# Optimization experiments

Hardware: AMD Instinct MI355X
Metric: run time of the kernel (lower is better)

The kernel has to match this reference:

```python
import jax, jax.numpy as jnp
import numpy as np

B, S, IN_DIM, CTX = 32, 512, 256, 128
D, H, L = 128, 4, 2
DH = D // H
HID = 512
TOTAL = 11 * D * D + 8 * D  # hypernet flat weight size per sample
EPS = 1e-5


def _layernorm(x, g, b):
    mu = jnp.mean(x, axis=-1, keepdims=True)
    var = jnp.mean(jnp.square(x - mu), axis=-1, keepdims=True)
    return (x - mu) * jax.lax.rsqrt(var + EPS) * g + b


def setup_inputs() -> dict:
    key = jax.random.key(0)
    ks = jax.random.split(key, 24)
    f32 = jnp.float32
    inp = {
        'x': jax.random.normal(ks[0], (B, S, IN_DIM), f32),
        'context_vector': jax.random.normal(ks[1], (B, CTX), f32),
        'in_proj_w': jax.random.normal(ks[2], (D, IN_DIM), f32) * (IN_DIM ** -0.5),
        'in_proj_b': jnp.zeros((D,), f32),
        'pe': jax.random.normal(ks[3], (1, S, D), f32) * 0.02,
        'hfc1_w': jax.random.normal(ks[4], (L, HID, CTX), f32) * (CTX ** -0.5),
        'hfc1_b': jnp.zeros((L, HID), f32),
        'hfc2_w': jax.random.normal(ks[5], (L, TOTAL, HID), f32) * 0.02,
        'hfc2_b': jnp.zeros((L, TOTAL), f32),
        'out_proj_w': jax.random.normal(ks[6], (L, D, D), f32) * (D ** -0.5),
        'out_proj_b': jnp.zeros((L, D), f32),
        'ln1_g': jnp.ones((L, D), f32), 'ln1_b': jnp.zeros((L, D), f32),
        'ln2_g': jnp.ones((L, D), f32), 'ln2_b': jnp.zeros((L, D), f32),
        'alpha1': jnp.full((L,), 0.5, f32), 'alpha2': jnp.full((L,), 0.5, f32),
        'head_w': jax.random.normal(ks[7], (1, D), f32) * (D ** -0.5),
        'head_b': jnp.zeros((1,), f32),
    }
    return inp


def reference(x, context_vector, in_proj_w, in_proj_b, pe, hfc1_w, hfc1_b,
              hfc2_w, hfc2_b, out_proj_w, out_proj_b, ln1_g, ln1_b,
              ln2_g, ln2_b, alpha1, alpha2, head_w, head_b):
    # input projection + learned positional encoding
    h = jnp.einsum('bsi,di->bsd', x, in_proj_w) + in_proj_b
    h = h + pe[:, :h.shape[1], :]

    # flat split offsets for hypernet output
    sizes = [3 * D * D, 3 * D, 4 * D * D, 4 * D, 4 * D * D, D]
    offs = np.concatenate([[0], np.cumsum(sizes)])

    for l in range(L):
        # hypernet: per-sample weights from context
        hid = jax.nn.relu(context_vector @ hfc1_w[l].T + hfc1_b[l])
        flat = hid @ hfc2_w[l].T + hfc2_b[l]  # [B, TOTAL]
        aw = flat[:, offs[0]:offs[1]].reshape(B, 3 * D, D)
        ab = flat[:, offs[1]:offs[2]]                     # [B, 3D]
        f1w = flat[:, offs[2]:offs[3]].reshape(B, 4 * D, D)
        f1b = flat[:, offs[3]:offs[4]]                    # [B, 4D]
        f2w = flat[:, offs[4]:offs[5]].reshape(B, D, 4 * D)
        f2b = flat[:, offs[5]:offs[6]]                    # [B, D]

        # per-sample QKV projection (grouped GEMM over batch)
        qkv = jnp.einsum('bsd,bed->bse', h, aw) + ab[:, None, :]
        q, k, v = jnp.split(qkv, 3, axis=-1)
        q = q.reshape(B, S, H, DH)
        k = k.reshape(B, S, H, DH)
        v = v.reshape(B, S, H, DH)
        scores = jnp.einsum('bqhd,bkhd->bhqk', q, k) / jnp.sqrt(jnp.float32(DH))
        attn = jax.nn.softmax(scores, axis=-1)
        ctx = jnp.einsum('bhqk,bkhd->bqhd', attn, v).reshape(B, S, D)
        attn_out = jnp.einsum('bsd,ed->bse', ctx, out_proj_w[l]) + out_proj_b[l]

        h = _layernorm(h + alpha1[l] * attn_out, ln1_g[l], ln1_b[l])

        # per-sample FFN
        ff = jax.nn.relu(jnp.einsum('bsd,bfd->bsf', h, f1w) + f1b[:, None, :])
        ff = jnp.einsum('bsf,bdf->bsd', ff, f2w) + f2b[:, None, :]

        h = _layernorm(h + alpha2[l] * ff, ln2_g[l], ln2_b[l])

    out = h[:, -1, :] @ head_w.T + head_b  # [B, 1]
    return out
```

## Files before the change

kernel.cpp:

```cpp
#include <hip/hip_runtime.h>
#include <hip/hip_bf16.h>

constexpr int B_    = 32;
constexpr int S_    = 512;
constexpr int INDIM = 256;
constexpr int KCTX  = 128;
constexpr int D_    = 128;
constexpr int H_    = 4;
constexpr int L_    = 2;
constexpr int HID_  = 512;
constexpr int TOTAL_ = 11 * D_ * D_ + 8 * D_;
constexpr int OFF_AB  = 3 * D_ * D_;
constexpr int OFF_F1W = OFF_AB + 3 * D_;
constexpr int OFF_F1B = OFF_F1W + 4 * D_ * D_;
constexpr int OFF_F2W = OFF_F1B + 4 * D_;
constexpr int OFF_F2B = OFF_F2W + 4 * D_ * D_;

typedef __attribute__((ext_vector_type(8))) short short8;
typedef __attribute__((ext_vector_type(4))) short short4v;
typedef __attribute__((ext_vector_type(2))) short short2v;
typedef __attribute__((ext_vector_type(4))) float f32x4;

#define MFMA16 __builtin_amdgcn_mfma_f32_16x16x32_bf16

__device__ __forceinline__ short f2bf(float f) {
  __hip_bfloat16 h = __float2bfloat16(f);
  return __builtin_bit_cast(short, h);
}
__device__ __forceinline__ float bf2f(short s) {
  __hip_bfloat16 h = __builtin_bit_cast(__hip_bfloat16, s);
  return __bfloat162float(h);
}
struct bfpair { short hi, lo; };
__device__ __forceinline__ bfpair split2p(float x) {
  bfpair p;
  p.hi = f2bf(x);
  p.lo = f2bf(x - bf2f(p.hi));
  return p;
}

__device__ __forceinline__ long ftaddr(int row, int k, int K) {
  return ((long)(row >> 4) * (K >> 3) + (k >> 3)) * 128 + (row & 15) * 8 + (k & 7);
}

__global__ void k_cvtft(const float* __restrict__ in, short* __restrict__ oh,
                        short* __restrict__ ol, int ktShift, int n8) {
  int t = blockIdx.x * 256 + threadIdx.x;
  if (t >= n8) return;
  int kt = 1 << ktShift;
  int row = t >> ktShift;
  int kc = t & (kt - 1);
  const float* p = in + ((long)row << (ktShift + 3)) + kc * 8;
  float4 v0 = *(const float4*)p;
  float4 v1 = *(const float4*)(p + 4);
  short8 h8, l8;
  bfpair q;
  q = split2p(v0.x); h8[0] = q.hi; l8[0] = q.lo;
  q = split2p(v0.y); h8[1] = q.hi; l8[1] = q.lo;
  q = split2p(v0.z); h8[2] = q.hi; l8[2] = q.lo;
  q = split2p(v0.w); h8[3] = q.hi; l8[3] = q.lo;
  q = split2p(v1.x); h8[4] = q.hi; l8[4] = q.lo;
  q = split2p(v1.y); h8[5] = q.hi; l8[5] = q.lo;
  q = split2p(v1.z); h8[6] = q.hi; l8[6] = q.lo;
  q = split2p(v1.w); h8[7] = q.hi; l8[7] = q.lo;
  long o = ((long)(row >> 4) * kt + kc) * 128 + (row & 15) * 8;
  *(short8*)(oh + o) = h8;
  *(short8*)(ol + o) = l8;
}

__global__ __launch_bounds__(512) void k_hid(const float* __restrict__ cvec,
                                             const float* __restrict__ w,
                                             const float* __restrict__ bias,
                                             short* __restrict__ hh,
                                             short* __restrict__ hl) {
  int lb = blockIdx.x;
  int b  = lb & 31;
  int j  = threadIdx.x;
  __shared__ float cs[KCTX];
  if (j < KCTX) cs[j] = cvec[b * KCTX + j];
  __syncthreads();
  int l = lb >> 5;
  const float* wr = w + (long)(l * HID_ + j) * KCTX;
  float s = bias[l * HID_ + j];
  #pragma unroll
  for (int c = 0; c < KCTX; c += 4) {
    float4 cv = *(const float4*)(cs + c);
    float4 wv = *(const float4*)(wr + c);
    s += cv.x * wv.x + cv.y * wv.y + cv.z * wv.z + cv.w * wv.w;
  }
  s = fmaxf(s, 0.f);
  bfpair p = split2p(s);
  long o = (long)l * 32 * HID_ + ((long)(b >> 4) * 64 + (j >> 3)) * 128 + (b & 15) * 8 + (j & 7);
  hh[o] = p.hi;
  hl[o] = p.lo;
}

__device__ __forceinline__ void store_flat(int b, int trow, float v,
    short* __restrict__ awh, short* __restrict__ awl,
    short* __restrict__ f1h, short* __restrict__ f1l,
    short* __restrict__ f2h, short* __restrict__ f2l,
    float* __restrict__ ab, float* __restrict__ f1b, float* __restrict__ f2b) {
  if (trow < OFF_AB) {
    int e = trow >> 7, d = trow & 127;
    long a = (long)b * 49152 + ftaddr(e, d, 128);
    bfpair p = split2p(v); awh[a] = p.hi; awl[a] = p.lo;
  } else if (trow < OFF_F1W) {
    ab[b * 384 + trow - OFF_AB] = v;
  } else if (trow < OFF_F1B) {
    int i = trow - OFF_F1W; int f = i >> 7, d = i & 127;
    long a = (long)b * 65536 + ftaddr(f, d, 128);
    bfpair p = split2p(v); f1h[a] = p.hi; f1l[a] = p.lo;
  } else if (trow < OFF_F2W) {
    f1b[b * 512 + trow - OFF_F1B] = v;
  } else if (trow < OFF_F2B) {
    int i = trow - OFF_F2W; int dd = i >> 9, f = i & 511;
    long a = (long)b * 65536 + ftaddr(dd, f, 512);
    bfpair p = split2p(v); f2h[a] = p.hi; f2l[a] = p.lo;
  } else {
    f2b[b * 128 + trow - OFF_F2B] = v;
  }
}

__global__ __launch_bounds__(256) void k_flat(
    const short* __restrict__ hidh, const short* __restrict__ hidl,
    const float* __restrict__ W, const float* __restrict__ bias,
    short* __restrict__ awh, short* __restrict__ awl,
    short* __restrict__ f1h, short* __restrict__ f1l,
    short* __restrict__ f2h, short* __restrict__ f2l,
    float* __restrict__ ab, float* __restrict__ f1b, float* __restrict__ f2b) {
  __shared__ short wls[2][64 * 64];
  const int tid = threadIdx.x, wave = tid >> 6, lane = tid & 63;
  const int r = lane & 15, g = lane >> 4;
  const int nb0 = blockIdx.x * 64;
  const int rr = tid >> 4;
  const int cc = (tid & 15) * 4;
  const float* wbase = W + (long)nb0 * HID_;
  float4 wv[2][4];
  #pragma unroll
  for (int rnd = 0; rnd < 4; ++rnd) {
    wv[0][rnd] = *(const float4*)(wbase + (long)(rnd * 16 + rr) * HID_ + cc);
    wv[1][rnd] = *(const float4*)(wbase + (long)(rnd * 16 + rr) * HID_ + 64 + cc);
  }
  const short* pAh = hidh + g * 128 + r * 8;
  const short* pAl = hidl + g * 128 + r * 8;
  f32x4 acc0 = {0, 0, 0, 0}, acc1 = {0, 0, 0, 0};
  int cur = 0;
  for (int c0 = 0; c0 < 512; c0 += 64) {
    #pragma unroll
    for (int rnd = 0; rnd < 4; ++rnd) {
      int row = rnd * 16 + rr;
      short4v h4, l4; bfpair q;
      q = split2p(wv[cur][rnd].x); h4[0] = q.hi; l4[0] = q.lo;
      q = split2p(wv[cur][rnd].y); h4[1] = q.hi; l4[1] = q.lo;
      q = split2p(wv[cur][rnd].z); h4[2] = q.hi; l4[2] = q.lo;
      q = split2p(wv[cur][rnd].w); h4[3] = q.hi; l4[3] = q.lo;
      int sb = row * 128 + ((cc * 2) ^ ((row & 7) << 4));
      *(short4v*)((char*)&wls[0][0] + sb) = h4;
      *(short4v*)((char*)&wls[1][0] + sb) = l4;
    }
    if (c0 + 128 < 512) {
      #pragma unroll
      for (int rnd = 0; rnd < 4; ++rnd)
        wv[cur][rnd] = *(const float4*)(wbase + (long)(rnd * 16 + rr) * HID_ + (c0 + 128) + cc);
    }
    __syncthreads();
    #pragma unroll
    for (int kk = 0; kk < 2; ++kk) {
      long ao = (long)(c0 * 16) + kk * 512;
      short8 ah0 = *(const short8*)(pAh + ao);
      short8 ah1 = *(const short8*)(pAh + 8192 + ao);
      short8 al0 = *(const short8*)(pAl + ao);
      short8 al1 = *(const short8*)(pAl + 8192 + ao);
      int wrow = wave * 16 + r;
      int wb = wrow * 128 + ((kk * 64 + g * 16) ^ ((r & 7) << 4));
      short8 wh = *(const short8*)((char*)&wls[0][0] + wb);
      short8 wl = *(const short8*)((char*)&wls[1][0] + wb);
      acc0 = MFMA16(ah0, wl, acc0, 0, 0, 0);
      acc0 = MFMA16(al0, wh, acc0, 0, 0, 0);
      acc0 = MFMA16(ah0, wh, acc0, 0, 0, 0);
      acc1 = MFMA16(ah1, wl, acc1, 0, 0, 0);
      acc1 = MFMA16(al1, wh, acc1, 0, 0, 0);
      acc1 = MFMA16(ah1, wh, acc1, 0, 0, 0);
    }
    __syncthreads();
    cur ^= 1;
  }
  int trow = nb0 + wave * 16 + r;
  float bv = bias[trow];
  #pragma unroll
  for (int reg = 0; reg < 4; ++reg) {
    store_flat(g * 4 + reg, trow, acc0[reg] + bv, awh, awl, f1h, f1l, f2h, f2l, ab, f1b, f2b);
    store_flat(g * 4 + reg + 16, trow, acc1[reg] + bv, awh, awl, f1h, f1l, f2h, f2l, ab, f1b, f2b);
  }
}

template <int K, int EPI, bool RELU>
__global__ __launch_bounds__(256) void k_gemm(
    const short* __restrict__ Ah, const short* __restrict__ Al, long sA,
    const short* __restrict__ Wh, const short* __restrict__ Wl, long sW,
    const float* __restrict__ biasP, long sB,
    void* __restrict__ p0, void* __restrict__ p1,
    void* __restrict__ p2, void* __restrict__ p3,
    const float* __restrict__ pe, int N,
    const float* __restrict__ lng, const float* __restrict__ lnb,
    const float* __restrict__ lnal) {
  extern __shared__ char smem_dyn[];
  const int tid = threadIdx.x, wave = tid >> 6, lane = tid & 63;
  const int r = lane & 15, g = lane >> 4;
  const int b = blockIdx.z;
  const int m0 = blockIdx.x * 64 + (wave & 1) * 32;
  const int n0 = blockIdx.y * 128 + (wave >> 1) * 64;
  const long KT = (long)K * 16;
  const short* pAh = Ah + (long)b * sA + (m0 >> 4) * KT + g * 128 + r * 8;
  const short* pAl = Al + (long)b * sA + (m0 >> 4) * KT + g * 128 + r * 8;
  const short* pWh = Wh + (long)b * sW + (n0 >> 4) * KT + g * 128 + r * 8;
  const short* pWl = Wl + (long)b * sW + (n0 >> 4) * KT + g * 128 + r * 8;
  f32x4 acc[2][4] = {{{0,0,0,0},{0,0,0,0},{0,0,0,0},{0,0,0,0}},
                     {{0,0,0,0},{0,0,0,0},{0,0,0,0},{0,0,0,0}}};
  for (int kk = 0; kk < K / 32; ++kk) {
    long ko = (long)kk * 512;
    short8 a0h = *(const short8*)(pAh + ko);
    short8 a1h = *(const short8*)(pAh + KT + ko);
    short8 a0l = *(const short8*)(pAl + ko);
    short8 a1l = *(const short8*)(pAl + KT + ko);
    #pragma unroll
    for (int ns = 0; ns < 4; ++ns) {
      short8 wh = *(const short8*)(pWh + ns * KT + ko);
      short8 wl = *(const short8*)(pWl + ns * KT + ko);
      acc[0][ns] = MFMA16(a0h, wl, acc[0][ns], 0, 0, 0);
      acc[0][ns] = MFMA16(a0l, wh, acc[0][ns], 0, 0, 0);
      acc[0][ns] = MFMA16(a0h, wh, acc[0][ns], 0, 0, 0);
      acc[1][ns] = MFMA16(a1h, wl, acc[1][ns], 0, 0, 0);
      acc[1][ns] = MFMA16(a1l, wh, acc[1][ns], 0, 0, 0);
      acc[1][ns] = MFMA16(a1h, wh, acc[1][ns], 0, 0, 0);
    }
  }
  #pragma unroll
  for (int ms = 0; ms < 2; ++ms) {
    #pragma unroll
    for (int ns = 0; ns < 4; ++ns) {
      int ccol = n0 + ns * 16 + r;
      float bv = biasP[(long)b * sB + ccol];
      #pragma unroll
      for (int reg = 0; reg < 4; ++reg) {
        int crow = m0 + ms * 16 + g * 4 + reg;
        float v = acc[ms][ns][reg] + bv;
        if constexpr (RELU) v = fmaxf(v, 0.f);
        if constexpr (EPI == 0) {
          long o = (long)b * 512 * N + (long)(crow >> 4) * (N * 16)
                 + (long)(ccol >> 3) * 128 + (crow & 15) * 8 + (ccol & 7);
          bfpair sp = split2p(v);
          ((short*)p0)[o] = sp.hi;
          ((short*)p1)[o] = sp.lo;
        } else if constexpr (EPI == 1) {
          v += pe[crow * D_ + ccol];
          ((float*)p0)[((long)b * S_ + crow) * D_ + ccol] = v;
          long o = (long)b * 65536 + (long)(crow >> 4) * 2048
                 + (ccol >> 3) * 128 + (crow & 15) * 8 + (ccol & 7);
          bfpair sp = split2p(v);
          ((short*)p1)[o] = sp.hi;
          ((short*)p2)[o] = sp.lo;
        } else if constexpr (EPI == 4) {
          float* tile = (float*)smem_dyn;
          int trow2 = (wave & 1) * 32 + ms * 16 + g * 4 + reg;
          int tcol = (wave >> 1) * 64 + ns * 16 + r;
          tile[trow2 * 136 + tcol] = v;
        } else {
          bfpair sp = split2p(v);
          if (n0 < 256) {
            long o = (long)b * 131072 + (long)(crow >> 4) * 4096
                   + (ccol >> 3) * 128 + (crow & 15) * 8 + (ccol & 7);
            ((short*)p0)[o] = sp.hi;
            ((short*)p1)[o] = sp.lo;
          } else {
            int c2 = ccol - 256; int hd = c2 >> 5, dd = c2 & 31;
            long o = (long)(b * 4 + hd) * 16384 + (dd >> 4) * 8192
                   + (crow >> 3) * 128 + (dd & 15) * 8 + (crow & 7);
            ((short*)p2)[o] = sp.hi;
            ((short*)p3)[o] = sp.lo;
          }
        }
      }
    }
  }
  if constexpr (EPI == 4) {
    float* tile = (float*)smem_dyn;
    __syncthreads();
    int row = tid >> 2, q = tid & 3;
    int brow = blockIdx.x * 64 + row;
    float a = lnal[0];
    float* hf = (float*)p0;
    float* hrow = hf + ((long)b * S_ + brow) * D_ + q * 32;
    float tv[32];
    float s = 0.f, ss = 0.f;
    #pragma unroll
    for (int i = 0; i < 32; i += 4) {
      float4 hv = *(const float4*)(hrow + i);
      float4 yv = *(const float4*)&tile[row * 136 + q * 32 + i];
      float t0 = hv.x + a * yv.x, t1 = hv.y + a * yv.y;
      float t2 = hv.z + a * yv.z, t3 = hv.w + a * yv.w;
      tv[i] = t0; tv[i+1] = t1; tv[i+2] = t2; tv[i+3] = t3;
      s += t0 + t1 + t2 + t3;
      ss += t0*t0 + t1*t1 + t2*t2 + t3*t3;
    }
    s  += __shfl_xor(s, 1);  s  += __shfl_xor(s, 2);
    ss += __shfl_xor(ss, 1); ss += __shfl_xor(ss, 2);
    float mu = s * (1.f / 128.f);
    float varv = ss * (1.f / 128.f) - mu * mu;
    float inv = rsqrtf(varv + 1e-5f);
    short* ph = (short*)p1; short* pl = (short*)p2;
    long fb = (long)b * 65536 + (long)(brow >> 4) * 2048 + (brow & 15) * 8;
    #pragma unroll
    for (int j = 0; j < 4; ++j) {
      short8 hv8, lv8;
      #pragma unroll
      for (int e = 0; e < 8; e += 4) {
        int i = j * 8 + e;
        int c = q * 32 + i;
        float4 gv = *(const float4*)(lng + c);
        float4 bb = *(const float4*)(lnb + c);
        float4 o4;
        o4.x = (tv[i]   - mu) * inv * gv.x + bb.x;
        o4.y = (tv[i+1] - mu) * inv * gv.y + bb.y;
        o4.z = (tv[i+2] - mu) * inv * gv.z + bb.z;
        o4.w = (tv[i+3] - mu) * inv * gv.w + bb.w;
        *(float4*)(hrow + i) = o4;
        bfpair q0 = split2p(o4.x); hv8[e]   = q0.hi; lv8[e]   = q0.lo;
        bfpair q1 = split2p(o4.y); hv8[e+1] = q1.hi; lv8[e+1] = q1.lo;
        bfpair q2 = split2p(o4.z); hv8[e+2] = q2.hi; lv8[e+2] = q2.lo;
        bfpair q3 = split2p(o4.w); hv8[e+3] = q3.hi; lv8[e+3] = q3.lo;
      }
      long o = fb + (q * 4 + j) * 128;
      *(short8*)(ph + o) = hv8;
      *(short8*)(pl + o) = lv8;
    }
  }
}

__global__ __launch_bounds__(128) void k_attn(const short* __restrict__ qkh,
                                              const short* __restrict__ qkl,
                                              const short* __restrict__ vth,
                                              const short* __restrict__ vtl,
                                              short* __restrict__ ch,
                                              short* __restrict__ cl) {
  __shared__ __align__(16) float scr[16][516];
  __shared__ __align__(16) float obuf[16][34];
  const int tid = threadIdx.x, wave = tid >> 6, lane = tid & 63;
  const int r = lane & 15, g = lane >> 4;
  const int b = blockIdx.z, hh = blockIdx.y;
  const int m0 = blockIdx.x * 16;
  const long qb = (long)b * 131072;
  const long qoff = qb + (long)(m0 >> 4) * 4096 + (hh * 4 + g) * 128 + r * 8;
  short8 qh = *(const short8*)(qkh + qoff);
  short8 ql = *(const short8*)(qkl + qoff);
  const float sc = 0.17677669529663687f;
  for (int n0 = wave * 256; n0 < wave * 256 + 256; n0 += 16) {
    long koff = qb + (long)(n0 >> 4) * 4096 + (16 + hh * 4 + g) * 128 + r * 8;
    short8 kh = *(const short8*)(qkh + koff);
    short8 kl = *(const short8*)(qkl + koff);
    f32x4 s = {0, 0, 0, 0};
    s = MFMA16(qh, kl, s, 0, 0, 0);
    s = MFMA16(ql, kh, s, 0, 0, 0);
    s = MFMA16(qh, kh, s, 0, 0, 0);
    #pragma unroll
    for (int reg = 0; reg < 4; ++reg)
      scr[g * 4 + reg][n0 + r] = s[reg] * sc;
  }
  __syncthreads();
  for (int row = wave * 8; row < wave * 8 + 8; ++row) {
    float v[8];
    #pragma unroll
    for (int i = 0; i < 8; ++i) v[i] = scr[row][lane + i * 64];
    float m = v[0];
    #pragma unroll
    for (int i = 1; i < 8; ++i) m = fmaxf(m, v[i]);
    #pragma unroll
    for (int o = 32; o > 0; o >>= 1) m = fmaxf(m, __shfl_xor(m, o));
    float ssum = 0.f;
    #pragma unroll
    for (int i = 0; i < 8; ++i) { v[i] = __expf(v[i] - m); ssum += v[i]; }
    #pragma unroll
    for (int o = 32; o > 0; o >>= 1) ssum += __shfl_xor(ssum, o);
    float inv = 1.f / ssum;
    #pragma unroll
    for (int i = 0; i < 8; ++i) scr[row][lane + i * 64] = v[i] * inv;
  }
  __syncthreads();
  f32x4 o0 = {0, 0, 0, 0}, o1 = {0, 0, 0, 0};
  const long vb = (long)(b * 4 + hh) * 16384;
  for (int kt = wave * 8; kt < wave * 8 + 8; ++kt) {
    float4 pv0 = *(const float4*)&scr[r][kt * 32 + g * 8];
    float4 pv1 = *(const float4*)&scr[r][kt * 32 + g * 8 + 4];
    short8 pah, pal;
    bfpair p;
    p = split2p(pv0.x); pah[0] = p.hi; pal[0] = p.lo;
    p = split2p(pv0.y); pah[1] = p.hi; pal[1] = p.lo;
    p = split2p(pv0.z); pah[2] = p.hi; pal[2] = p.lo;
    p = split2p(pv0.w); pah[3] = p.hi; pal[3] = p.lo;
    p = split2p(pv1.x); pah[4] = p.hi; pal[4] = p.lo;
    p = split2p(pv1.y); pah[5] = p.hi; pal[5] = p.lo;
    p = split2p(pv1.z); pah[6] = p.hi; pal[6] = p.lo;
    p = split2p(pv1.w); pah[7] = p.hi; pal[7] = p.lo;
    long vo = vb + (long)(kt * 4 + g) * 128 + r * 8;
    short8 vh0 = *(const short8*)(vth + vo);
    short8 vh1 = *(const short8*)(vth + vo + 8192);
    short8 vl0 = *(const short8*)(vtl + vo);
    short8 vl1 = *(const short8*)(vtl + vo + 8192);
    o0 = MFMA16(pah, vl0, o0, 0, 0, 0);
    o0 = MFMA16(pal, vh0, o0, 0, 0, 0);
    o0 = MFMA16(pah, vh0, o0, 0, 0, 0);
    o1 = MFMA16(pah, vl1, o1, 0, 0, 0);
    o1 = MFMA16(pal, vh1, o1, 0, 0, 0);
    o1 = MFMA16(pah, vh1, o1, 0, 0, 0);
  }
  if (wave == 1) {
    #pragma unroll
    for (int reg = 0; reg < 4; ++reg) {
      obuf[g * 4 + reg][r] = o0[reg];
      obuf[g * 4 + reg][17 + r] = o1[reg];
    }
  }
  __syncthreads();
  if (wave == 0) {
    #pragma unroll
    for (int reg = 0; reg < 4; ++reg) {
      float a0 = o0[reg] + obuf[g * 4 + reg][r];
      float a1 = o1[reg] + obuf[g * 4 + reg][17 + r];
      int srow = m0 + g * 4 + reg;
      int col0 = hh * 32 + r;
      long o = (long)b * 65536 + (long)(srow >> 4) * 2048
             + (col0 >> 3) * 128 + (srow & 15) * 8 + (col0 & 7);
      bfpair sp0 = split2p(a0);
      ch[o] = sp0.hi; cl[o] = sp0.lo;
      long o2 = o + 2 * 128;
      bfpair sp1 = split2p(a1);
      ch[o2] = sp1.hi; cl[o2] = sp1.lo;
    }
  }
}

__global__ __launch_bounds__(64) void k_head(const float* __restrict__ h,
                                             const float* __restrict__ hw,
                                             const float* __restrict__ hb,
                                             float* __restrict__ out) {
  int b = blockIdx.x, lane = threadIdx.x;
  const float* hr = h + ((long)b * S_ + (S_ - 1)) * D_;
  float v = hr[lane] * hw[lane] + hr[lane + 64] * hw[lane + 64];
  #pragma unroll
  for (int o = 32; o > 0; o >>= 1) v += __shfl_xor(v, o);
  if (lane == 0) out[b] = v + hb[0];
}

extern "C" void kernel_launch(void* const* d_in, const int* in_sizes, int n_in,
                              void* d_out, int out_size, void* d_ws, size_t ws_size,
                              hipStream_t stream) {
  const float* x    = (const float*)d_in[0];
  const float* cvec = (const float*)d_in[1];
  const float* ipw  = (const float*)d_in[2];
  const float* ipb  = (const float*)d_in[3];
  const float* pe   = (const float*)d_in[4];
  const float* h1w  = (const float*)d_in[5];
  const float* h1b  = (const float*)d_in[6];
  const float* h2w  = (const float*)d_in[7];
  const float* h2b  = (const float*)d_in[8];
  const float* opw  = (const float*)d_in[9];
  const float* opb  = (const float*)d_in[10];
  const float* ln1g = (const float*)d_in[11];
  const float* ln1b = (const float*)d_in[12];
  const float* ln2g = (const float*)d_in[13];
  const float* ln2b = (const float*)d_in[14];
  const float* a1   = (const float*)d_in[15];
  const float* a2   = (const float*)d_in[16];
  const float* hw   = (const float*)d_in[17];
  const float* hb   = (const float*)d_in[18];
  float* out = (float*)d_out;

  char* ws = (char*)d_ws;
  size_t off = 0;
  auto alloc = [&](size_t n) { void* p = ws + off; off = (off + n + 255) & ~(size_t)255; return p; };

  short* ff1h  = (short*)alloc((size_t)B_ * S_ * 512 * 2);
  short* ff1l  = (short*)alloc((size_t)B_ * S_ * 512 * 2);
  short* xFh   = ff1h;
  short* xFl   = ff1l;
  float* h_f   = (float*)alloc((size_t)B_ * S_ * D_ * 4);
  short* hFh   = (short*)alloc((size_t)B_ * S_ * D_ * 2);
  short* hFl   = (short*)alloc((size_t)B_ * S_ * D_ * 2);
  short* hidFh = (short*)alloc((size_t)L_ * 32 * HID_ * 2);
  short* hidFl = (short*)alloc((size_t)L_ * 32 * HID_ * 2);
  short* awFh  = (short*)alloc((size_t)B_ * 49152 * 2);
  short* awFl  = (short*)alloc((size_t)B_ * 49152 * 2);
  short* f1wFh = (short*)alloc((size_t)B_ * 65536 * 2);
  short* f1wFl = (short*)alloc((size_t)B_ * 65536 * 2);
  short* f2wFh = (short*)alloc((size_t)B_ * 65536 * 2);
  short* f2wFl = (short*)alloc((size_t)B_ * 65536 * 2);
  float* abF   = (float*)alloc((size_t)B_ * 384 * 4);
  float* f1bF  = (float*)alloc((size_t)B_ * 512 * 4);
  float* f2bF  = (float*)alloc((size_t)B_ * 128 * 4);
  short* qkFh  = (short*)alloc((size_t)B_ * S_ * 256 * 2);
  short* qkFl  = (short*)alloc((size_t)B_ * S_ * 256 * 2);
  short* vtFh  = (short*)alloc((size_t)B_ * H_ * 32 * S_ * 2);
  short* vtFl  = (short*)alloc((size_t)B_ * H_ * 32 * S_ * 2);
  short* cxFh  = (short*)alloc((size_t)B_ * S_ * D_ * 2);
  short* cxFl  = (short*)alloc((size_t)B_ * S_ * D_ * 2);
  short* ipwFh = (short*)alloc((size_t)D_ * INDIM * 2);
  short* ipwFl = (short*)alloc((size_t)D_ * INDIM * 2);
  short* opwFh = (short*)alloc((size_t)L_ * D_ * D_ * 2);
  short* opwFl = (short*)alloc((size_t)L_ * D_ * D_ * 2);

  k_cvtft<<<(B_ * S_ * INDIM / 8 + 255) / 256, 256, 0, stream>>>(x, xFh, xFl, 5, B_ * S_ * INDIM / 8);
  k_cvtft<<<16, 256, 0, stream>>>(ipw, ipwFh, ipwFl, 5, D_ * INDIM / 8);
  k_cvtft<<<16, 256, 0, stream>>>(opw, opwFh, opwFl, 4, L_ * D_ * D_ / 8);

  k_hid<<<L_ * 32, 512, 0, stream>>>(cvec, h1w, h1b, hidFh, hidFl);

  k_gemm<INDIM, 1, false><<<dim3(8, 1, B_), 256, 0, stream>>>(
      xFh, xFl, (long)S_ * INDIM, ipwFh, ipwFl, 0, ipb, 0,
      h_f, hFh, hFl, nullptr, pe, 128, nullptr, nullptr, nullptr);

  constexpr size_t LN_LDS = 64 * 136 * 4;
  for (int l = 0; l < L_; ++l) {
    k_flat<<<TOTAL_ / 64, 256, 0, stream>>>(
        hidFh + (long)l * 32 * HID_, hidFl + (long)l * 32 * HID_,
        h2w + (long)l * TOTAL_ * HID_, h2b + (long)l * TOTAL_,
        awFh, awFl, f1wFh, f1wFl, f2wFh, f2wFl, abF, f1bF, f2bF);
    k_gemm<D_, 5, false><<<dim3(8, 3, B_), 256, 0, stream>>>(
        hFh, hFl, (long)S_ * D_, awFh, awFl, 49152, abF, 384,
        qkFh, qkFl, vtFh, vtFl, nullptr, 256, nullptr, nullptr, nullptr);
    k_attn<<<dim3(S_ / 16, H_, B_), 128, 0, stream>>>(qkFh, qkFl, vtFh, vtFl, cxFh, cxFl);
    k_gemm<D_, 4, false><<<dim3(8, 1, B_), 256, LN_LDS, stream>>>(
        cxFh, cxFl, (long)S_ * D_, opwFh + l * 16384, opwFl + l * 16384, 0,
        opb + l * D_, 0, h_f, hFh, hFl, nullptr, nullptr, 128,
        ln1g + l * D_, ln1b + l * D_, a1 + l);
    k_gemm<D_, 0, true><<<dim3(8, 4, B_), 256, 0, stream>>>(
        hFh, hFl, (long)S_ * D_, f1wFh, f1wFl, 65536, f1bF, 512,
        ff1h, ff1l, nullptr, nullptr, nullptr, 512, nullptr, nullptr, nullptr);
    k_gemm<512, 4, false><<<dim3(8, 1, B_), 256, LN_LDS, stream>>>(
        ff1h, ff1l, (long)S_ * 512, f2wFh, f2wFl, 65536, f2bF, 128,
        h_f, hFh, hFl, nullptr, nullptr, 128,
        ln2g + l * D_, ln2b + l * D_, a2 + l);
  }
  k_head<<<B_, 64, 0, stream>>>(h_f, hw, hb, out);
}
```

Before: 513.1 us.

## Load hypernet weights directly into MFMA fragments, dropping LDS staging and barriers

The hypernet output GEMM kernel no longer stages fp32 weight tiles through shared memory with swizzling and two barriers per chunk. Each lane now loads its own 8 contiguous weights per K-step straight from global memory, with a one-step register prefetch, splits them into bf16 hi/lo, and feeds them to the MFMAs. This removes LDS traffic and synchronisation in a kernel that streams a large weight matrix once. The cost is less coalesced global access: each lane reads 32 bytes from a separate row, so every access touches many rows at once.

```diff
diff --git a/kernel.cpp b/kernel.cpp
--- a/kernel.cpp
+++ b/kernel.cpp
@@ -128,69 +128,55 @@
     short* __restrict__ f1h, short* __restrict__ f1l,
     short* __restrict__ f2h, short* __restrict__ f2l,
     float* __restrict__ ab, float* __restrict__ f1b, float* __restrict__ f2b) {
-  __shared__ short wls[2][64 * 64];
   const int tid = threadIdx.x, wave = tid >> 6, lane = tid & 63;
   const int r = lane & 15, g = lane >> 4;
   const int nb0 = blockIdx.x * 64;
-  const int rr = tid >> 4;
-  const int cc = (tid & 15) * 4;
-  const float* wbase = W + (long)nb0 * HID_;
-  float4 wv[2][4];
-  #pragma unroll
-  for (int rnd = 0; rnd < 4; ++rnd) {
-    wv[0][rnd] = *(const float4*)(wbase + (long)(rnd * 16 + rr) * HID_ + cc);
-    wv[1][rnd] = *(const float4*)(wbase + (long)(rnd * 16 + rr) * HID_ + 64 + cc);
-  }
+  const int wrow = nb0 + wave * 16 + r;
+  const float* wp = W + (long)wrow * HID_ + g * 8;
   const short* pAh = hidh + g * 128 + r * 8;
   const short* pAl = hidl + g * 128 + r * 8;
   f32x4 acc0 = {0, 0, 0, 0}, acc1 = {0, 0, 0, 0};
-  int cur = 0;
-  for (int c0 = 0; c0 < 512; c0 += 64) {
-    #pragma unroll
-    for (int rnd = 0; rnd < 4; ++rnd) {
-      int row = rnd * 16 + rr;
-      short4v h4, l4; bfpair q;
-      q = split2p(wv[cur][rnd].x); h4[0] = q.hi; l4[0] = q.lo;
-      q = split2p(wv[cur][rnd].y); h4[1] = q.hi; l4[1] = q.lo;
-      q = split2p(wv[cur][rnd].z); h4[2] = q.hi; l4[2] = q.lo;
-      q = split2p(wv[cur][rnd].w); h4[3] = q.hi; l4[3] = q.lo;
-      int sb = row * 128 + ((cc * 2) ^ ((row & 7) << 4));
-      *(short4v*)((char*)&wls[0][0] + sb) = h4;
-      *(short4v*)((char*)&wls[1][0] + sb) = l4;
-    }
-    if (c0 + 128 < 512) {
-      #pragma unroll
-      for (int rnd = 0; rnd < 4; ++rnd)
-        wv[cur][rnd] = *(const float4*)(wbase + (long)(rnd * 16 + rr) * HID_ + (c0 + 128) + cc);
-    }
-    __syncthreads();
-    #pragma unroll
-    for (int kk = 0; kk < 2; ++kk) {
-      long ao = (long)(c0 * 16) + kk * 512;
-      short8 ah0 = *(const short8*)(pAh + ao);
-      short8 ah1 = *(const short8*)(pAh + 8192 + ao);
-      short8 al0 = *(const short8*)(pAl + ao);
-      short8 al1 = *(const short8*)(pAl + 8192 + ao);
-      int wrow = wave * 16 + r;
-      int wb = wrow * 128 + ((kk * 64 + g * 16) ^ ((r & 7) << 4));
-      short8 wh = *(const short8*)((char*)&wls[0][0] + wb);
-      short8 wl = *(const short8*)((char*)&wls[1][0] + wb);
-      acc0 = MFMA16(ah0, wl, acc0, 0, 0, 0);
-      acc0 = MFMA16(al0, wh, acc0, 0, 0, 0);
-      acc0 = MFMA16(ah0, wh, acc0, 0, 0, 0);
-      acc1 = MFMA16(ah1, wl, acc1, 0, 0, 0);
-      acc1 = MFMA16(al1, wh, acc1, 0, 0, 0);
-      acc1 = MFMA16(ah1, wh, acc1, 0, 0, 0);
-    }
-    __syncthreads();
-    cur ^= 1;
-  }
-  int trow = nb0 + wave * 16 + r;
-  float bv = bias[trow];
+  float4 w0 = *(const float4*)(wp);
+  float4 w1 = *(const float4*)(wp + 4);
+  short8 ah0 = *(const short8*)(pAh);
+  short8 ah1 = *(const short8*)(pAh + 8192);
+  short8 al0 = *(const short8*)(pAl);
+  short8 al1 = *(const short8*)(pAl + 8192);
+  #pragma unroll
+  for (int kk = 0; kk < 16; ++kk) {
+    float4 cw0 = w0, cw1 = w1;
+    short8 ch0 = ah0, ch1 = ah1, cl0 = al0, cl1 = al1;
+    if (kk < 15) {
+      long wo = (long)(kk + 1) * 32;
+      w0 = *(const float4*)(wp + wo);
+      w1 = *(const float4*)(wp + wo + 4);
+      long ao = (long)(kk + 1) * 512;
+      ah0 = *(const short8*)(pAh + ao);
+      ah1 = *(const short8*)(pAh + 8192 + ao);
+      al0 = *(const short8*)(pAl + ao);
+      al1 = *(const short8*)(pAl + 8192 + ao);
+    }
+    short8 wh, wl; bfpair q;
+    q = split2p(cw0.x); wh[0] = q.hi; wl[0] = q.lo;
+    q = split2p(cw0.y); wh[1] = q.hi; wl[1] = q.lo;
+    q = split2p(cw0.z); wh[2] = q.hi; wl[2] = q.lo;
+    q = split2p(cw0.w); wh[3] = q.hi; wl[3] = q.lo;
+    q = split2p(cw1.x); wh[4] = q.hi; wl[4] = q.lo;
+    q = split2p(cw1.y); wh[5] = q.hi; wl[5] = q.lo;
+    q = split2p(cw1.z); wh[6] = q.hi; wl[6] = q.lo;
+    q = split2p(cw1.w); wh[7] = q.hi; wl[7] = q.lo;
+    acc0 = MFMA16(ch0, wl, acc0, 0, 0, 0);
+    acc0 = MFMA16(cl0, wh, acc0, 0, 0, 0);
+    acc0 = MFMA16(ch0, wh, acc0, 0, 0, 0);
+    acc1 = MFMA16(ch1, wl, acc1, 0, 0, 0);
+    acc1 = MFMA16(cl1, wh, acc1, 0, 0, 0);
+    acc1 = MFMA16(ch1, wh, acc1, 0, 0, 0);
+  }
+  float bv = bias[wrow];
   #pragma unroll
   for (int reg = 0; reg < 4; ++reg) {
-    store_flat(g * 4 + reg, trow, acc0[reg] + bv, awh, awl, f1h, f1l, f2h, f2l, ab, f1b, f2b);
-    store_flat(g * 4 + reg + 16, trow, acc1[reg] + bv, awh, awl, f1h, f1l, f2h, f2l, ab, f1b, f2b);
+    store_flat(g * 4 + reg, wrow, acc0[reg] + bv, awh, awl, f1h, f1l, f2h, f2l, ab, f1b, f2b);
+    store_flat(g * 4 + reg + 16, wrow, acc1[reg] + bv, awh, awl, f1h, f1l, f2h, f2l, ab, f1b, f2b);
   }
 }
 
```

Measured after the change: 558.2 us. 1.09x slower.

## Batch both hypernet layers in one launch and vectorize GEMM epilogue stores

Applied to the files above, without the earlier changes.

The two per-layer hypernet weight-generation launches become one launch with a layer grid dimension, and the generated weights are stored per layer in larger workspace buffers. The GEMM epilogue for the QKV and FFN1 outputs now stages results through an LDS tile and writes 8-wide vectorized bf16 hi/lo stores instead of scattered scalar stores. The V-transpose part is written with 4-wide vector stores. The LDS tile pitch changes from 136 to 132 floats. This adds LDS traffic and a barrier to those GEMMs and doubles the weight workspace.

```diff
diff --git a/kernel.cpp b/kernel.cpp
--- a/kernel.cpp
+++ b/kernel.cpp
@@ -15,6 +15,7 @@
 constexpr int OFF_F1B = OFF_F1W + 4 * D_ * D_;
 constexpr int OFF_F2W = OFF_F1B + 4 * D_;
 constexpr int OFF_F2B = OFF_F2W + 4 * D_ * D_;
+constexpr int TP = 132;
 
 typedef __attribute__((ext_vector_type(8))) short short8;
 typedef __attribute__((ext_vector_type(4))) short short4v;
@@ -129,6 +130,15 @@
     short* __restrict__ f2h, short* __restrict__ f2l,
     float* __restrict__ ab, float* __restrict__ f1b, float* __restrict__ f2b) {
   __shared__ short wls[2][64 * 64];
+  const int l = blockIdx.y;
+  hidh += (long)l * 32 * HID_;
+  hidl += (long)l * 32 * HID_;
+  W    += (long)l * TOTAL_ * HID_;
+  bias += (long)l * TOTAL_;
+  awh  += (long)l * B_ * 49152;  awl += (long)l * B_ * 49152;
+  f1h  += (long)l * B_ * 65536;  f1l += (long)l * B_ * 65536;
+  f2h  += (long)l * B_ * 65536;  f2l += (long)l * B_ * 65536;
+  ab   += l * B_ * 384;  f1b += l * B_ * 512;  f2b += l * B_ * 128;
   const int tid = threadIdx.x, wave = tid >> 6, lane = tid & 63;
   const int r = lane & 15, g = lane >> 4;
   const int nb0 = blockIdx.x * 64;
@@ -235,57 +245,99 @@
       acc[1][ns] = MFMA16(a1h, wh, acc[1][ns], 0, 0, 0);
     }
   }
-  #pragma unroll
-  for (int ms = 0; ms < 2; ++ms) {
-    #pragma unroll
-    for (int ns = 0; ns < 4; ++ns) {
-      int ccol = n0 + ns * 16 + r;
-      float bv = biasP[(long)b * sB + ccol];
+
+  if constexpr (EPI == 5) {
+    if (blockIdx.y == 2) {
       #pragma unroll
-      for (int reg = 0; reg < 4; ++reg) {
-        int crow = m0 + ms * 16 + g * 4 + reg;
-        float v = acc[ms][ns][reg] + bv;
-        if constexpr (RELU) v = fmaxf(v, 0.f);
-        if constexpr (EPI == 0) {
-          long o = (long)b * 512 * N + (long)(crow >> 4) * (N * 16)
-                 + (long)(ccol >> 3) * 128 + (crow & 15) * 8 + (ccol & 7);
-          bfpair sp = split2p(v);
-          ((short*)p0)[o] = sp.hi;
-          ((short*)p1)[o] = sp.lo;
-        } else if constexpr (EPI == 1) {
-          v += pe[crow * D_ + ccol];
+      for (int ms = 0; ms < 2; ++ms) {
+        int crow0 = m0 + ms * 16 + g * 4;
+        #pragma unroll
+        for (int ns = 0; ns < 4; ++ns) {
+          int ccol = n0 + ns * 16 + r;
+          float bv = biasP[(long)b * sB + ccol];
+          int c2 = ccol - 256, hd = c2 >> 5, dd = c2 & 31;
+          short4v h4, l4; bfpair q;
+          #pragma unroll
+          for (int reg = 0; reg < 4; ++reg) {
+            float v = acc[ms][ns][reg] + bv;
+            q = split2p(v); h4[reg] = q.hi; l4[reg] = q.lo;
+          }
+          long o = (long)(b * 4 + hd) * 16384 + (dd >> 4) * 8192
+                 + (crow0 >> 3) * 128 + (dd & 15) * 8 + (crow0 & 7);
+          *(short4v*)((short*)p2 + o) = h4;
+          *(short4v*)((short*)p3 + o) = l4;
+        }
+      }
+      return;
+    }
+  }
+
+  if constexpr (EPI == 1) {
+    #pragma unroll
+    for (int ms = 0; ms < 2; ++ms) {
+      #pragma unroll
+      for (int ns = 0; ns < 4; ++ns) {
+        int ccol = n0 + ns * 16 + r;
+        float bv = biasP[ccol];
+        #pragma unroll
+        for (int reg = 0; reg < 4; ++reg) {
+          int crow = m0 + ms * 16 + g * 4 + reg;
+          float v = acc[ms][ns][reg] + bv + pe[crow * D_ + ccol];
           ((float*)p0)[((long)b * S_ + crow) * D_ + ccol] = v;
           long o = (long)b * 65536 + (long)(crow >> 4) * 2048
                  + (ccol >> 3) * 128 + (crow & 15) * 8 + (ccol & 7);
           bfpair sp = split2p(v);
           ((short*)p1)[o] = sp.hi;
           ((short*)p2)[o] = sp.lo;
-        } else if constexpr (EPI == 4) {
-          float* tile = (float*)smem_dyn;
-          int trow2 = (wave & 1) * 32 + ms * 16 + g * 4 + reg;
-          int tcol = (wave >> 1) * 64 + ns * 16 + r;
-          tile[trow2 * 136 + tcol] = v;
-        } else {
-          bfpair sp = split2p(v);
-          if (n0 < 256) {
-            long o = (long)b * 131072 + (long)(crow >> 4) * 4096
-                   + (ccol >> 3) * 128 + (crow & 15) * 8 + (ccol & 7);
-            ((short*)p0)[o] = sp.hi;
-            ((short*)p1)[o] = sp.lo;
-          } else {
-            int c2 = ccol - 256; int hd = c2 >> 5, dd = c2 & 31;
-            long o = (long)(b * 4 + hd) * 16384 + (dd >> 4) * 8192
-                   + (crow >> 3) * 128 + (dd & 15) * 8 + (crow & 7);
-            ((short*)p2)[o] = sp.hi;
-            ((short*)p3)[o] = sp.lo;
-          }
         }
       }
     }
-  }
-  if constexpr (EPI == 4) {
-    float* tile = (float*)smem_dyn;
-    __syncthreads();
+    return;
+  }
+
+  float* tile = (float*)smem_dyn;
+  #pragma unroll
+  for (int ms = 0; ms < 2; ++ms) {
+    #pragma unroll
+    for (int ns = 0; ns < 4; ++ns) {
+      int ccol = n0 + ns * 16 + r;
+      float bv = biasP[(long)b * sB + ccol];
+      #pragma unroll
+      for (int reg = 0; reg < 4; ++reg) {
+        float v = acc[ms][ns][reg] + bv;
+        if constexpr (RELU) v = fmaxf(v, 0.f);
+        int trow2 = (wave & 1) * 32 + ms * 16 + g * 4 + reg;
+        int tcol = (wave >> 1) * 64 + ns * 16 + r;
+        tile[trow2 * TP + tcol] = v;
+      }
+    }
+  }
+  __syncthreads();
+
+  if constexpr (EPI == 0 || EPI == 5) {
+    int row = tid >> 2, cg = tid & 3;
+    int crow = blockIdx.x * 64 + row;
+    long rowbase = (long)b * 512 * N + (long)(crow >> 4) * (16 * (long)N) + (crow & 15) * 8;
+    #pragma unroll
+    for (int j4 = 0; j4 < 4; ++j4) {
+      int tcol = j4 * 32 + cg * 8;
+      float4 aa = *(const float4*)&tile[row * TP + tcol];
+      float4 bb = *(const float4*)&tile[row * TP + tcol + 4];
+      short8 h8, l8; bfpair q;
+      q = split2p(aa.x); h8[0] = q.hi; l8[0] = q.lo;
+      q = split2p(aa.y); h8[1] = q.hi; l8[1] = q.lo;
+      q = split2p(aa.z); h8[2] = q.hi; l8[2] = q.lo;
+      q = split2p(aa.w); h8[3] = q.hi; l8[3] = q.lo;
+      q = split2p(bb.x); h8[4] = q.hi; l8[4] = q.lo;
+      q = split2p(bb.y); h8[5] = q.hi; l8[5] = q.lo;
+      q = split2p(bb.z); h8[6] = q.hi; l8[6] = q.lo;
+      q = split2p(bb.w); h8[7] = q.hi; l8[7] = q.lo;
+      int ccol = blockIdx.y * 128 + tcol;
+      long o = rowbase + (long)(ccol >> 3) * 128;
+      *(short8*)((short*)p0 + o) = h8;
+      *(short8*)((short*)p1 + o) = l8;
+    }
+  } else if constexpr (EPI == 4) {
     int row = tid >> 2, q = tid & 3;
     int brow = blockIdx.x * 64 + row;
     float a = lnal[0];
@@ -296,7 +348,7 @@
     #pragma unroll
     for (int i = 0; i < 32; i += 4) {
       float4 hv = *(const float4*)(hrow + i);
-      float4 yv = *(const float4*)&tile[row * 136 + q * 32 + i];
+      float4 yv = *(const float4*)&tile[row * TP + q * 32 + i];
       float t0 = hv.x + a * yv.x, t1 = hv.y + a * yv.y;
       float t2 = hv.z + a * yv.z, t3 = hv.w + a * yv.w;
       tv[i] = t0; tv[i+1] = t1; tv[i+2] = t2; tv[i+3] = t3;
@@ -479,6 +531,10 @@
   size_t off = 0;
   auto alloc = [&](size_t n) { void* p = ws + off; off = (off + n + 255) & ~(size_t)255; return p; };
 
+  const long AWs = (long)B_ * 49152;
+  const long F1s = (long)B_ * 65536;
+  const long F2s = (long)B_ * 65536;
+
   short* ff1h  = (short*)alloc((size_t)B_ * S_ * 512 * 2);
   short* ff1l  = (short*)alloc((size_t)B_ * S_ * 512 * 2);
   short* xFh   = ff1h;
@@ -488,15 +544,15 @@
   short* hFl   = (short*)alloc((size_t)B_ * S_ * D_ * 2);
   short* hidFh = (short*)alloc((size_t)L_ * 32 * HID_ * 2);
   short* hidFl = (short*)alloc((size_t)L_ * 32 * HID_ * 2);
-  short* awFh  = (short*)alloc((size_t)B_ * 49152 * 2);
-  short* awFl  = (short*)alloc((size_t)B_ * 49152 * 2);
-  short* f1wFh = (short*)alloc((size_t)B_ * 65536 * 2);
-  short* f1wFl = (short*)alloc((size_t)B_ * 65536 * 2);
-  short* f2wFh = (short*)alloc((size_t)B_ * 65536 * 2);
-  short* f2wFl = (short*)alloc((size_t)B_ * 65536 * 2);
-  float* abF   = (float*)alloc((size_t)B_ * 384 * 4);
-  float* f1bF  = (float*)alloc((size_t)B_ * 512 * 4);
-  float* f2bF  = (float*)alloc((size_t)B_ * 128 * 4);
+  short* awFh  = (short*)alloc((size_t)L_ * AWs * 2);
+  short* awFl  = (short*)alloc((size_t)L_ * AWs * 2);
+  short* f1wFh = (short*)alloc((size_t)L_ * F1s * 2);
+  short* f1wFl = (short*)alloc((size_t)L_ * F1s * 2);
+  short* f2wFh = (short*)alloc((size_t)L_ * F2s * 2);
+  short* f2wFl = (short*)alloc((size_t)L_ * F2s * 2);
+  float* abF   = (float*)alloc((size_t)L_ * B_ * 384 * 4);
+  float* f1bF  = (float*)alloc((size_t)L_ * B_ * 512 * 4);
+  float* f2bF  = (float*)alloc((size_t)L_ * B_ * 128 * 4);
   short* qkFh  = (short*)alloc((size_t)B_ * S_ * 256 * 2);
   short* qkFl  = (short*)alloc((size_t)B_ * S_ * 256 * 2);
   short* vtFh  = (short*)alloc((size_t)B_ * H_ * 32 * S_ * 2);
@@ -514,29 +570,32 @@
 
   k_hid<<<L_ * 32, 512, 0, stream>>>(cvec, h1w, h1b, hidFh, hidFl);
 
+  k_flat<<<dim3(TOTAL_ / 64, 2), 256, 0, stream>>>(
+      hidFh, hidFl, h2w, h2b, awFh, awFl, f1wFh, f1wFl, f2wFh, f2wFl,
+      abF, f1bF, f2bF);
+
   k_gemm<INDIM, 1, false><<<dim3(8, 1, B_), 256, 0, stream>>>(
       xFh, xFl, (long)S_ * INDIM, ipwFh, ipwFl, 0, ipb, 0,
       h_f, hFh, hFl, nullptr, pe, 128, nullptr, nullptr, nullptr);
 
-  constexpr size_t LN_LDS = 64 * 136 * 4;
+  constexpr size_t TILE_LDS = 64 * TP * 4;
   for (int l = 0; l < L_; ++l) {
-    k_flat<<<TOTAL_ / 64, 256, 0, stream>>>(
-        hidFh + (long)l * 32 * HID_, hidFl + (long)l * 32 * HID_,
-        h2w + (long)l * TOTAL_ * HID_, h2b + (long)l * TOTAL_,
-        awFh, awFl, f1wFh, f1wFl, f2wFh, f2wFl, abF, f1bF, f2bF);
-    k_gemm<D_, 5, false><<<dim3(8, 3, B_), 256, 0, stream>>>(
-        hFh, hFl, (long)S_ * D_, awFh, awFl, 49152, abF, 384,
+    k_gemm<D_, 5, false><<<dim3(8, 3, B_), 256, TILE_LDS, stream>>>(
+        hFh, hFl, (long)S_ * D_, awFh + l * AWs, awFl + l * AWs, 49152,
+        abF + l * B_ * 384, 384,
         qkFh, qkFl, vtFh, vtFl, nullptr, 256, nullptr, nullptr, nullptr);
     k_attn<<<dim3(S_ / 16, H_, B_), 128, 0, stream>>>(qkFh, qkFl, vtFh, vtFl, cxFh, cxFl);
-    k_gemm<D_, 4, false><<<dim3(8, 1, B_), 256, LN_LDS, stream>>>(
+    k_gemm<D_, 4, false><<<dim3(8, 1, B_), 256, TILE_LDS, stream>>>(
         cxFh, cxFl, (long)S_ * D_, opwFh + l * 16384, opwFl + l * 16384, 0,
         opb + l * D_, 0, h_f, hFh, hFl, nullptr, nullptr, 128,
         ln1g + l * D_, ln1b + l * D_, a1 + l);
-    k_gemm<D_, 0, true><<<dim3(8, 4, B_), 256, 0, stream>>>(
-        hFh, hFl, (long)S_ * D_, f1wFh, f1wFl, 65536, f1bF, 512,
+    k_gemm<D_, 0, true><<<dim3(8, 4, B_), 256, TILE_LDS, stream>>>(
+        hFh, hFl, (long)S_ * D_, f1wFh + l * F1s, f1wFl + l * F1s, 65536,
+        f1bF + l * B_ * 512, 512,
         ff1h, ff1l, nullptr, nullptr, nullptr, 512, nullptr, nullptr, nullptr);
-    k_gemm<512, 4, false><<<dim3(8, 1, B_), 256, LN_LDS, stream>>>(
-        ff1h, ff1l, (long)S_ * 512, f2wFh, f2wFl, 65536, f2bF, 128,
+    k_gemm<512, 4, false><<<dim3(8, 1, B_), 256, TILE_LDS, stream>>>(
+        ff1h, ff1l, (long)S_ * 512, f2wFh + l * F2s, f2wFl + l * F2s, 65536,
+        f2bF + l * B_ * 128, 128,
         h_f, hFh, hFl, nullptr, nullptr, 128,
         ln2g + l * D_, ln2b + l * D_, a2 + l);
   }
```

After: 506.1 us. Within noise of the previous version (-1.4%).
